# Performance work log

Measured on AMD Instinct MI355X. Metric: run time of the kernel, lower is better.

## Reference

```python
import jax, jax.numpy as jnp
import numpy as np

B, H, W, C = 8, 64, 64, 384
HEADS, WS = 12, 14
KD = C // HEADS          # key_dim = 32
D = KD                    # attn_ratio = 1 -> d = key_dim
DH = D * HEADS            # = 384
HID = 4 * C               # mlp hidden = 1536
SCALE = KD ** -0.5
EPS = 1e-5
N = WS * WS               # 196 tokens per window


def _bias_idx():
    pts = [(i, j) for i in range(WS) for j in range(WS)]
    off, idxs = {}, []
    for p1 in pts:
        for p2 in pts:
            o = (abs(p1[0] - p2[0]), abs(p1[1] - p2[1]))
            if o not in off:
                off[o] = len(off)
            idxs.append(off[o])
    return np.asarray(idxs, np.int32).reshape(N, N), len(off)


def setup_inputs() -> dict:
    key = jax.random.key(0)
    ks = jax.random.split(key, 8)
    bias_idx_np, n_off = _bias_idx()  # n_off == 196 for a 14x14 window
    s = 0.02
    return {
        "x": jax.random.normal(ks[0], (B, H * W, C), jnp.float32),
        "ln_attn_w": jnp.ones((C,), jnp.float32),
        "ln_attn_b": jnp.zeros((C,), jnp.float32),
        "qkv_w": jax.random.normal(ks[1], (3 * DH, C), jnp.float32) * s,
        "qkv_b": jnp.zeros((3 * DH,), jnp.float32),
        "proj_w": jax.random.normal(ks[2], (C, DH), jnp.float32) * s,
        "proj_b": jnp.zeros((C,), jnp.float32),
        "attn_biases": jax.random.normal(ks[3], (HEADS, n_off), jnp.float32) * s,
        "conv_w": jax.random.normal(ks[4], (C, 1, 3, 3), jnp.float32) * s,  # depthwise OIHW
        "bn_w": jnp.ones((C,), jnp.float32),
        "bn_b": jnp.zeros((C,), jnp.float32),
        "bn_mean": jnp.zeros((C,), jnp.float32),
        "bn_var": jnp.ones((C,), jnp.float32),
        "ln_mlp_w": jnp.ones((C,), jnp.float32),
        "ln_mlp_b": jnp.zeros((C,), jnp.float32),
        "fc1_w": jax.random.normal(ks[5], (HID, C), jnp.float32) * s,
        "fc1_b": jnp.zeros((HID,), jnp.float32),
        "fc2_w": jax.random.normal(ks[6], (C, HID), jnp.float32) * s,
        "fc2_b": jnp.zeros((C,), jnp.float32),
        "bias_idx": jnp.asarray(bias_idx_np),
    }


def _ln(x, w, b):
    m = jnp.mean(x, -1, keepdims=True)
    v = jnp.mean((x - m) ** 2, -1, keepdims=True)
    return (x - m) * jax.lax.rsqrt(v + EPS) * w + b


def reference(x, ln_attn_w, ln_attn_b, qkv_w, qkv_b, proj_w, proj_b, attn_biases,
              conv_w, bn_w, bn_b, bn_mean, bn_var, ln_mlp_w, ln_mlp_b,
              fc1_w, fc1_b, fc2_w, fc2_b, bias_idx):
    L = H * W
    res = x
    # ---- window partition (pad 64 -> 70, 5x5 windows of 14x14) ----
    pad = (-H) % WS
    pH = H + pad
    n = pH // WS
    xw = x.reshape(B, H, W, C)
    xw = jnp.pad(xw, ((0, 0), (0, pad), (0, pad), (0, 0)))
    xw = xw.reshape(B, n, WS, n, WS, C).transpose(0, 1, 3, 2, 4, 5)
    xw = xw.reshape(B * n * n, N, C)
    # ---- attention with relative-position bias ----
    xn = _ln(xw, ln_attn_w, ln_attn_b)
    qkv = xn @ qkv_w.T + qkv_b                       # [Bw, N, 3*DH]
    qkv = qkv.reshape(-1, N, HEADS, 3 * KD)
    q, k, v = qkv[..., :KD], qkv[..., KD:2 * KD], qkv[..., 2 * KD:]
    bias = attn_biases[:, bias_idx]                  # [HEADS, N, N]
    attn = jnp.einsum('bnhd,bmhd->bhnm', q, k) * SCALE + bias[None]
    attn = jax.nn.softmax(attn, axis=-1)
    out = jnp.einsum('bhnm,bmhd->bnhd', attn, v).reshape(-1, N, DH)
    out = out @ proj_w.T + proj_b
    # ---- window reverse + crop + residual ----
    out = out.reshape(B, n, n, WS, WS, C).transpose(0, 1, 3, 2, 4, 5)
    out = out.reshape(B, pH, pH, C)[:, :H, :W]
    x = res + out.reshape(B, L, C)
    # ---- depthwise local conv + BN (eval mode) ----
    xc = x.reshape(B, H, W, C).transpose(0, 3, 1, 2)  # NCHW
    xc = jax.lax.conv_general_dilated(xc, conv_w, (1, 1), 'SAME',
                                      feature_group_count=C)
    inv = jax.lax.rsqrt(bn_var + 1e-5)
    xc = (xc - bn_mean[None, :, None, None]) * (inv * bn_w)[None, :, None, None] \
         + bn_b[None, :, None, None]
    x = xc.reshape(B, C, L).transpose(0, 2, 1)
    # ---- MLP (LN -> fc1 -> GELU(exact) -> fc2) + residual ----
    h = _ln(x, ln_mlp_w, ln_mlp_b)
    h = jax.nn.gelu(h @ fc1_w.T + fc1_b, approximate=False)
    h = h @ fc2_w.T + fc2_b
    return x + h
```

## Files before the change

### kernel.cpp

```cpp
#include <hip/hip_runtime.h>
#include <hip/hip_bf16.h>

#define DI __device__ __forceinline__

typedef __attribute__((ext_vector_type(8))) __bf16 bf16x8;
typedef __attribute__((ext_vector_type(4))) float f32x4;
typedef __attribute__((ext_vector_type(2))) float f32x2;
typedef __attribute__((ext_vector_type(8))) unsigned short us8;
typedef __attribute__((ext_vector_type(4))) unsigned short us4;

constexpr int CBATCH = 8;
constexpr int HW = 64;
constexpr int CDIM = 384;
constexpr int HEADS = 12;
constexpr int WS = 14;
constexpr int NTOK = 196;
constexpr int NWIN = 200;
constexpr int MV = 39200;
constexpr int MPAD = 39296;
constexpr int NQKV = 1152;
constexpr int HIDD = 1536;
constexpr int MMLP = 32768;
constexpr int NBIAS = 12 * 13 * 13 * 4 * 16 * 4;
constexpr int PLSTR = 228;
constexpr float SCALE = 0.17677669529663687f;

DI unsigned short f2bf(float f) { __bf16 b = (__bf16)f; return __builtin_bit_cast(unsigned short, b); }
DI bf16x8 ldfrag(const unsigned short* p) { return __builtin_bit_cast(bf16x8, *(const us8*)p); }
DI f32x4 mfma16(bf16x8 a, bf16x8 b, f32x4 c) {
  return __builtin_amdgcn_mfma_f32_16x16x32_bf16(a, b, c, 0, 0, 0);
}
DI void async16(const void* g, void* l) {
  __builtin_amdgcn_global_load_lds((const __attribute__((address_space(1))) void*)g,
                                   (__attribute__((address_space(3))) void*)l, 16, 0, 0);
}
DI int vt_addr(int d, int t) {
  return d * 256 + (((t & ~7) ^ ((d & 7) << 3) ^ (((d >> 3) & 3) << 5)) | (t & 7));
}

__global__ __launch_bounds__(256) void k_cvt(const float* __restrict__ s,
                                             unsigned short* __restrict__ d, int n) {
  int i = blockIdx.x * 256 + threadIdx.x;
  if (i < n) d[i] = f2bf(s[i]);
}

__global__ __launch_bounds__(256) void k_bias2(const float* __restrict__ ab,
                                               const int* __restrict__ bidx,
                                               float* __restrict__ bt, int n_off) {
  int i = blockIdx.x * 256 + threadIdx.x;
  if (i >= NBIAS) return;
  int r = i & 3, l15 = (i >> 2) & 15, g = (i >> 6) & 3;
  int j = i >> 8;
  int kt = j % 13;
  int j2 = j / 13;
  int qt = j2 % 13;
  int h = j2 / 13;
  int q = qt * 16 + l15, k = kt * 16 + g * 4 + r;
  float v = 0.f;
  if (q < 196 && k < 196) v = ab[h * n_off + bidx[q * 196 + k]];
  bt[i] = v;
}

template <int WIN>
__global__ __launch_bounds__(256) void k_ln(const float* __restrict__ src,
                                            const float* __restrict__ lw,
                                            const float* __restrict__ lb,
                                            unsigned short* __restrict__ dst) {
  const int row = blockIdx.x * 4 + (threadIdx.x >> 6);
  const int l = threadIdx.x & 63;
  const int c0 = l * 6;
  const float* p;
  bool valid;
  if (WIN) {
    int win = row / 196, t = row - win * 196;
    int b = win / 25, wi = win - b * 25;
    int wr = wi / 5, wc = wi - wr * 5;
    int hh = wr * 14 + t / 14, ww = wc * 14 + (t - (t / 14) * 14);
    valid = (row < MV) && (hh < HW) && (ww < HW);
    p = src + ((size_t)b * 4096 + hh * 64 + ww) * CDIM;
  } else {
    valid = true;
    p = src + (size_t)row * CDIM;
  }
  float v[6];
  if (valid) {
    f32x2 a = *(const f32x2*)(p + c0);
    f32x2 b2 = *(const f32x2*)(p + c0 + 2);
    f32x2 c2 = *(const f32x2*)(p + c0 + 4);
    v[0] = a.x; v[1] = a.y; v[2] = b2.x; v[3] = b2.y; v[4] = c2.x; v[5] = c2.y;
  } else {
#pragma unroll
    for (int k = 0; k < 6; ++k) v[k] = 0.f;
  }
  float s = 0.f, q = 0.f;
#pragma unroll
  for (int k = 0; k < 6; ++k) { s += v[k]; q += v[k] * v[k]; }
#pragma unroll
  for (int m = 1; m <= 32; m <<= 1) {
    s += __shfl_xor(s, m, 64);
    q += __shfl_xor(q, m, 64);
  }
  float mean = s * (1.0f / 384.0f);
  float var = q * (1.0f / 384.0f) - mean * mean;
  float rs = rsqrtf(var + 1e-5f);
#pragma unroll
  for (int k = 0; k < 6; ++k) {
    float y = (v[k] - mean) * rs * lw[c0 + k] + lb[c0 + k];
    dst[(size_t)row * CDIM + c0 + k] = f2bf(y);
  }
}

__global__ __launch_bounds__(256) void k_conv(const float* __restrict__ x1,
                                              const float* __restrict__ cw,
                                              const float* __restrict__ bw,
                                              const float* __restrict__ bb,
                                              const float* __restrict__ bm,
                                              const float* __restrict__ bv,
                                              float* __restrict__ x2) {
  int idx = blockIdx.x * 256 + threadIdx.x;
  int c = idx % 384;
  int x = (idx / 384) & 63;
  int b = idx / (384 * 64);
  const float* base = x1 + (size_t)b * 4096 * 384 + c;
  float w[9];
#pragma unroll
  for (int k = 0; k < 9; ++k) w[k] = cw[c * 9 + k];
  float sc = rsqrtf(bv[c] + 1e-5f) * bw[c];
  float sb = bb[c] - bm[c] * sc;
  float t0m = 0.f, t0c = 0.f, t0p = 0.f;
  float t1m, t1c, t1p, t2m, t2c, t2p;
  t1m = (x > 0) ? base[(x - 1) * 384] : 0.f;
  t1c = base[x * 384];
  t1p = (x < 63) ? base[(x + 1) * 384] : 0.f;
  for (int y = 0; y < 64; ++y) {
    if (y < 63) {
      int ro = (y + 1) * 64;
      t2m = (x > 0) ? base[(ro + x - 1) * 384] : 0.f;
      t2c = base[(ro + x) * 384];
      t2p = (x < 63) ? base[(ro + x + 1) * 384] : 0.f;
    } else { t2m = t2c = t2p = 0.f; }
    float o = w[0] * t0m + w[1] * t0c + w[2] * t0p +
              w[3] * t1m + w[4] * t1c + w[5] * t1p +
              w[6] * t2m + w[7] * t2c + w[8] * t2p;
    x2[((size_t)b * 4096 + y * 64 + x) * 384 + c] = o * sc + sb;
    t0m = t1m; t0c = t1c; t0p = t1p;
    t1m = t2m; t1c = t2c; t1p = t2p;
  }
}

__global__ __launch_bounds__(256, 4) void k_attn(const unsigned short* __restrict__ qkv,
                                                 const float* __restrict__ bias_f,
                                                 unsigned short* __restrict__ aout) {
  __shared__ unsigned short Vt[32 * 256];
  __shared__ unsigned short Pl[4][16 * PLSTR];
  const int bid = blockIdx.x;
  const int blk = (bid & 7) * 300 + (bid >> 3);
  const int win = blk / 12, h = blk - win * 12;
  const int tid = threadIdx.x;
  const int w = tid >> 6, l = tid & 63;
  const int l15 = l & 15, g = l >> 4;
  const unsigned short* qb = qkv + (size_t)win * 196 * 1152 + h * 96;

  for (int i = tid; i < 896; i += 256) {
    int t = i >> 2, d8 = (i & 3) << 3;
    us8 z = {0, 0, 0, 0, 0, 0, 0, 0};
    if (t < 196) z = *(const us8*)(qb + (size_t)t * 1152 + 64 + d8);
#pragma unroll
    for (int j = 0; j < 8; ++j) Vt[vt_addr(d8 + j, t)] = z[j];
  }
  for (int z = l; z < 16 * 20; z += 64) {
    int rr = z / 20, cc = 208 + (z - rr * 20);
    Pl[w][rr * PLSTR + cc] = 0;
  }
  __syncthreads();

  const float* bth = bias_f + (size_t)h * (13 * 13 * 4 * 16 * 4);
  unsigned short* plw = &Pl[w][0];
  for (int qt = w; qt < 13; qt += 4) {
    bf16x8 aq = ldfrag(qb + (size_t)(qt * 16 + l15) * 1152 + g * 8);
    float su = 0.f;
#pragma unroll
    for (int kt = 0; kt < 13; ++kt) {
      f32x4 zz = {0.f, 0.f, 0.f, 0.f};
      bf16x8 bk = ldfrag(qb + (size_t)(kt * 16 + l15) * 1152 + 32 + g * 8);
      f32x4 s = mfma16(bk, aq, zz);
      f32x4 bb = *(const f32x4*)(bth + (size_t)(((qt * 13 + kt) * 4 + g) * 16 + l15) * 4);
      us4 pk;
#pragma unroll
      for (int r = 0; r < 4; ++r) {
        float p = __expf(s[r] + bb[r]);
        if (kt == 12 && g != 0) p = 0.f;
        su += p;
        pk[r] = f2bf(p);
      }
      *(us4*)(plw + l15 * PLSTR + kt * 16 + g * 4) = pk;
    }
    su += __shfl_xor(su, 16, 64);
    su += __shfl_xor(su, 32, 64);
    asm volatile("s_waitcnt lgkmcnt(0)" ::: "memory");
    __builtin_amdgcn_sched_barrier(0);
    f32x4 o0 = {0.f, 0.f, 0.f, 0.f}, o1 = {0.f, 0.f, 0.f, 0.f};
#pragma unroll
    for (int kc = 0; kc < 7; ++kc) {
      int t0 = kc * 32 + g * 8;
      bf16x8 pa = ldfrag(plw + l15 * PLSTR + t0);
      bf16x8 b0 = ldfrag(&Vt[vt_addr(l15, t0)]);
      bf16x8 b1 = ldfrag(&Vt[vt_addr(16 + l15, t0)]);
      o0 = mfma16(pa, b0, o0);
      o1 = mfma16(pa, b1, o1);
    }
    float inv = 1.0f / su;
#pragma unroll
    for (int r = 0; r < 4; ++r) {
      int rw = qt * 16 + g * 4 + r;
      if (rw < 196) {
        size_t rb = ((size_t)win * 196 + rw) * 384 + h * 32;
        aout[rb + l15] = f2bf(o0[r] * inv);
        aout[rb + 16 + l15] = f2bf(o1[r] * inv);
      }
    }
  }
}

template <int MODE>
__global__ __launch_bounds__(256) void k_gemm(const unsigned short* __restrict__ A,
                                              const unsigned short* __restrict__ B,
                                              const float* __restrict__ bias,
                                              const float* __restrict__ auxr,
                                              float* __restrict__ auxw,
                                              unsigned short* __restrict__ outb,
                                              int K) {
  __shared__ unsigned short As[128 * 64];
  __shared__ unsigned short Bs[128 * 64];
  const int tid = threadIdx.x;
  const int w = tid >> 6, l = tid & 63;
  const int l15 = l & 15, g = l >> 4;
  const int wm = w >> 1, wn = w & 1;
  const size_t arow0 = (size_t)blockIdx.x * 128;
  const size_t brow0 = (size_t)blockIdx.y * 128;
  f32x4 acc[4][4] = {};
  for (int ks = 0; ks < K; ks += 64) {
    if (ks) __syncthreads();
#pragma unroll
    for (int it = 0; it < 4; ++it) {
      const int f = it * 256 + tid;
      const int r = f >> 3, c8 = (f & 7) << 3;
      const int lb = (it * 256 + w * 64) * 8;
      async16(A + (arow0 + r) * K + ks + c8, &As[lb]);
      async16(B + (brow0 + r) * K + ks + c8, &Bs[lb]);
    }
    __syncthreads();
#pragma unroll
    for (int kk = 0; kk < 2; ++kk) {
      bf16x8 af[4], bfr[4];
#pragma unroll
      for (int i = 0; i < 4; ++i)
        af[i] = ldfrag(&As[(wm * 64 + i * 16 + l15) * 64 + kk * 32 + g * 8]);
#pragma unroll
      for (int j = 0; j < 4; ++j)
        bfr[j] = ldfrag(&Bs[(wn * 64 + j * 16 + l15) * 64 + kk * 32 + g * 8]);
#pragma unroll
      for (int i = 0; i < 4; ++i)
#pragma unroll
        for (int j = 0; j < 4; ++j)
          acc[i][j] = mfma16(af[i], bfr[j], acc[i][j]);
    }
  }
#pragma unroll
  for (int i = 0; i < 4; ++i) {
#pragma unroll
    for (int j = 0; j < 4; ++j) {
#pragma unroll
      for (int r = 0; r < 4; ++r) {
        const int row = (int)arow0 + wm * 64 + i * 16 + g * 4 + r;
        const int col = (int)brow0 + wn * 64 + j * 16 + l15;
        float v = acc[i][j][r] + bias[col];
        if (MODE == 0) {
          int ch = col % 96;
          float o = (ch < 32) ? v * SCALE : v;
          outb[(size_t)row * NQKV + col] = f2bf(o);
        } else if (MODE == 1) {
          if (row < MV) {
            int win = row / 196, t = row - win * 196;
            int b = win / 25, wi = win - b * 25;
            int wr = wi / 5, wc = wi - wr * 5;
            int hh = wr * 14 + t / 14, ww = wc * 14 + (t - (t / 14) * 14);
            if (hh < HW && ww < HW) {
              size_t di = ((size_t)b * 4096 + hh * 64 + ww) * 384 + col;
              auxw[di] = auxr[di] + v;
            }
          }
        } else if (MODE == 2) {
          float gl = 0.5f * v * (1.0f + erff(v * 0.7071067811865475f));
          outb[(size_t)row * HIDD + col] = f2bf(gl);
        } else {
          size_t di = (size_t)row * 384 + col;
          auxw[di] = auxr[di] + v;
        }
      }
    }
  }
}

extern "C" void kernel_launch(void* const* d_in, const int* in_sizes, int n_in,
                              void* d_out, int out_size, void* d_ws, size_t ws_size,
                              hipStream_t stream) {
  const float* x = (const float*)d_in[0];
  const float* ln_attn_w = (const float*)d_in[1];
  const float* ln_attn_b = (const float*)d_in[2];
  const float* qkv_w = (const float*)d_in[3];
  const float* qkv_b = (const float*)d_in[4];
  const float* proj_w = (const float*)d_in[5];
  const float* proj_b = (const float*)d_in[6];
  const float* attn_biases = (const float*)d_in[7];
  const float* conv_w = (const float*)d_in[8];
  const float* bn_w = (const float*)d_in[9];
  const float* bn_b = (const float*)d_in[10];
  const float* bn_mean = (const float*)d_in[11];
  const float* bn_var = (const float*)d_in[12];
  const float* ln_mlp_w = (const float*)d_in[13];
  const float* ln_mlp_b = (const float*)d_in[14];
  const float* fc1_w = (const float*)d_in[15];
  const float* fc1_b = (const float*)d_in[16];
  const float* fc2_w = (const float*)d_in[17];
  const float* fc2_b = (const float*)d_in[18];
  const int* bias_idx = (const int*)d_in[19];

  char* ws = (char*)d_ws;
  size_t off = 0;
  auto alloc = [&](size_t n) {
    void* p = ws + off;
    off = (off + n + 255) & ~(size_t)255;
    return p;
  };
  unsigned short* xn = (unsigned short*)alloc((size_t)MPAD * CDIM * 2);
  unsigned short* qkv = (unsigned short*)alloc((size_t)MMLP * HIDD * 2);
  unsigned short* attn = (unsigned short*)alloc((size_t)MMLP * CDIM * 4);
  float* x1 = (float*)alloc((size_t)MMLP * CDIM * 4);
  unsigned short* wq = (unsigned short*)alloc((size_t)NQKV * CDIM * 2);
  unsigned short* wp = (unsigned short*)alloc((size_t)CDIM * CDIM * 2);
  unsigned short* w1 = (unsigned short*)alloc((size_t)HIDD * CDIM * 2);
  unsigned short* w2 = (unsigned short*)alloc((size_t)CDIM * HIDD * 2);
  float* bias_f = (float*)alloc((size_t)NBIAS * 4);
  unsigned short* hbuf = qkv;
  float* x2 = (float*)attn;
  unsigned short* xln = xn;
  int n_off = in_sizes[7] / HEADS;

  dim3 B256(256);
  k_cvt<<<dim3((NQKV * CDIM + 255) / 256), B256, 0, stream>>>(qkv_w, wq, NQKV * CDIM);
  k_cvt<<<dim3((CDIM * CDIM + 255) / 256), B256, 0, stream>>>(proj_w, wp, CDIM * CDIM);
  k_cvt<<<dim3((HIDD * CDIM + 255) / 256), B256, 0, stream>>>(fc1_w, w1, HIDD * CDIM);
  k_cvt<<<dim3((CDIM * HIDD + 255) / 256), B256, 0, stream>>>(fc2_w, w2, CDIM * HIDD);
  k_bias2<<<dim3((NBIAS + 255) / 256), B256, 0, stream>>>(attn_biases, bias_idx, bias_f, n_off);
  k_ln<1><<<dim3(MPAD / 4), B256, 0, stream>>>(x, ln_attn_w, ln_attn_b, xn);
  k_gemm<0><<<dim3(MPAD / 128, NQKV / 128), B256, 0, stream>>>(xn, wq, qkv_b, nullptr, nullptr, qkv, CDIM);
  k_attn<<<dim3(NWIN * HEADS), B256, 0, stream>>>(qkv, bias_f, attn);
  k_gemm<1><<<dim3(MPAD / 128, CDIM / 128), B256, 0, stream>>>(attn, wp, proj_b, x, x1, nullptr, CDIM);
  k_conv<<<dim3(CBATCH * HW * CDIM / 256), B256, 0, stream>>>(x1, conv_w, bn_w, bn_b, bn_mean, bn_var, x2);
  k_ln<0><<<dim3(MMLP / 4), B256, 0, stream>>>(x2, ln_mlp_w, ln_mlp_b, xln);
  k_gemm<2><<<dim3(MMLP / 128, HIDD / 128), B256, 0, stream>>>(xln, w1, fc1_b, nullptr, nullptr, hbuf, CDIM);
  k_gemm<3><<<dim3(MMLP / 128, CDIM / 128), B256, 0, stream>>>(hbuf, w2, fc2_b, x2, (float*)d_out, nullptr, HIDD);
}
```

Baseline: 617.2 us.

## Pass softmax probabilities through registers via ds_bpermute and XCD-remap GEMM blocks

```diff
diff --git a/kernel.cpp b/kernel.cpp
--- a/kernel.cpp
+++ b/kernel.cpp
@@ -8,6 +8,7 @@
 typedef __attribute__((ext_vector_type(2))) float f32x2;
 typedef __attribute__((ext_vector_type(8))) unsigned short us8;
 typedef __attribute__((ext_vector_type(4))) unsigned short us4;
+typedef __attribute__((ext_vector_type(4))) int i32x4;
 
 constexpr int CBATCH = 8;
 constexpr int HW = 64;
@@ -22,7 +23,6 @@
 constexpr int HIDD = 1536;
 constexpr int MMLP = 32768;
 constexpr int NBIAS = 12 * 13 * 13 * 4 * 16 * 4;
-constexpr int PLSTR = 228;
 constexpr float SCALE = 0.17677669529663687f;
 
 DI unsigned short f2bf(float f) { __bf16 b = (__bf16)f; return __builtin_bit_cast(unsigned short, b); }
@@ -152,7 +152,6 @@
                                                  const float* __restrict__ bias_f,
                                                  unsigned short* __restrict__ aout) {
   __shared__ unsigned short Vt[32 * 256];
-  __shared__ unsigned short Pl[4][16 * PLSTR];
   const int bid = blockIdx.x;
   const int blk = (bid & 7) * 300 + (bid >> 3);
   const int win = blk / 12, h = blk - win * 12;
@@ -168,42 +167,51 @@
 #pragma unroll
     for (int j = 0; j < 8; ++j) Vt[vt_addr(d8 + j, t)] = z[j];
   }
-  for (int z = l; z < 16 * 20; z += 64) {
-    int rr = z / 20, cc = 208 + (z - rr * 20);
-    Pl[w][rr * PLSTR + cc] = 0;
-  }
   __syncthreads();
 
   const float* bth = bias_f + (size_t)h * (13 * 13 * 4 * 16 * 4);
-  unsigned short* plw = &Pl[w][0];
+  const int pl1 = (l15 + ((l & 16) << 1)) << 2;
+  const int pl2 = pl1 + 64;
+
   for (int qt = w; qt < 13; qt += 4) {
     bf16x8 aq = ldfrag(qb + (size_t)(qt * 16 + l15) * 1152 + g * 8);
     float su = 0.f;
+    us4 pk[13];
 #pragma unroll
     for (int kt = 0; kt < 13; ++kt) {
       f32x4 zz = {0.f, 0.f, 0.f, 0.f};
       bf16x8 bk = ldfrag(qb + (size_t)(kt * 16 + l15) * 1152 + 32 + g * 8);
       f32x4 s = mfma16(bk, aq, zz);
       f32x4 bb = *(const f32x4*)(bth + (size_t)(((qt * 13 + kt) * 4 + g) * 16 + l15) * 4);
-      us4 pk;
 #pragma unroll
       for (int r = 0; r < 4; ++r) {
         float p = __expf(s[r] + bb[r]);
         if (kt == 12 && g != 0) p = 0.f;
         su += p;
-        pk[r] = f2bf(p);
+        pk[kt][r] = f2bf(p);
       }
-      *(us4*)(plw + l15 * PLSTR + kt * 16 + g * 4) = pk;
     }
     su += __shfl_xor(su, 16, 64);
     su += __shfl_xor(su, 32, 64);
-    asm volatile("s_waitcnt lgkmcnt(0)" ::: "memory");
-    __builtin_amdgcn_sched_barrier(0);
     f32x4 o0 = {0.f, 0.f, 0.f, 0.f}, o1 = {0.f, 0.f, 0.f, 0.f};
 #pragma unroll
     for (int kc = 0; kc < 7; ++kc) {
+      us4 sel;
+      if (kc < 6) {
+        sel = (g & 2) ? pk[2 * kc + 1] : pk[2 * kc];
+      } else {
+        us4 z4 = {0, 0, 0, 0};
+        sel = (g & 2) ? z4 : pk[12];
+      }
+      int sx = (int)(((unsigned)sel[0]) | ((unsigned)sel[1] << 16));
+      int sy = (int)(((unsigned)sel[2]) | ((unsigned)sel[3] << 16));
+      i32x4 pw;
+      pw[0] = __builtin_amdgcn_ds_bpermute(pl1, sx);
+      pw[1] = __builtin_amdgcn_ds_bpermute(pl1, sy);
+      pw[2] = __builtin_amdgcn_ds_bpermute(pl2, sx);
+      pw[3] = __builtin_amdgcn_ds_bpermute(pl2, sy);
+      bf16x8 pa = __builtin_bit_cast(bf16x8, pw);
       int t0 = kc * 32 + g * 8;
-      bf16x8 pa = ldfrag(plw + l15 * PLSTR + t0);
       bf16x8 b0 = ldfrag(&Vt[vt_addr(l15, t0)]);
       bf16x8 b1 = ldfrag(&Vt[vt_addr(16 + l15, t0)]);
       o0 = mfma16(pa, b0, o0);
@@ -236,8 +244,14 @@
   const int w = tid >> 6, l = tid & 63;
   const int l15 = l & 15, g = l >> 4;
   const int wm = w >> 1, wn = w & 1;
-  const size_t arow0 = (size_t)blockIdx.x * 128;
-  const size_t brow0 = (size_t)blockIdx.y * 128;
+  const int nwg = gridDim.x * gridDim.y;
+  const int orig = blockIdx.y * gridDim.x + blockIdx.x;
+  const int cq = nwg >> 3, cr = nwg & 7;
+  const int xcd = orig & 7, cidx = orig >> 3;
+  const int flat = (xcd < cr ? xcd * (cq + 1) : cr * (cq + 1) + (xcd - cr) * cq) + cidx;
+  const int bx = flat % gridDim.x, by = flat / gridDim.x;
+  const size_t arow0 = (size_t)bx * 128;
+  const size_t brow0 = (size_t)by * 128;
   f32x4 acc[4][4] = {};
   for (int ks = 0; ks < K; ks += 64) {
     if (ks) __syncthreads();
```

New measurement: 680.9 us. +10.3%, slower.
